# Kernel optimization log

Hardware: AMD Instinct MI355X
Metric: run time of the kernel (lower is better)

## Reference

```python
import jax, jax.numpy as jnp
import numpy as np

BN_EPS = 1e-5
NUM_GRAPHS = 64


def _gin_layer(x, src, dst, eps, w1, b1, gamma, beta, w2, b2):
    # GIN aggregation: sum of source features into destination nodes
    n = x.shape[0]
    agg = jax.ops.segment_sum(x[src], dst, num_segments=n)  # [N, d]
    h = (1.0 + eps) * x + agg
    # MLP: Linear -> BatchNorm1d (batch stats, train mode) -> ReLU -> Linear
    h = h @ w1 + b1
    mu = jnp.mean(h, axis=0)
    var = jnp.var(h, axis=0)
    h = gamma * (h - mu) * jax.lax.rsqrt(var + BN_EPS) + beta
    h = jax.nn.relu(h)
    return h @ w2 + b2


def setup_inputs() -> dict:
    key = jax.random.key(0)
    ks = jax.random.split(key, 16)
    N, E, F = 100000, 3200000, 128
    x = jax.random.normal(ks[0], (N, F), dtype=jnp.float32)
    edge_index = jax.random.randint(ks[1], (2, E), 0, N, dtype=jnp.int64)
    batch = jnp.sort(jax.random.randint(ks[2], (N,), 0, NUM_GRAPHS, dtype=jnp.int64))

    def lin(k, fin, fout):
        kw, kb = jax.random.split(k)
        s = 1.0 / np.sqrt(fin)
        w = jax.random.uniform(kw, (fin, fout), jnp.float32, -s, s)
        b = jax.random.uniform(kb, (fout,), jnp.float32, -s, s)
        return w, b

    w1a, b1a = lin(ks[3], F, 64)
    w1b, b1b = lin(ks[4], 64, 32)
    w2a, b2a = lin(ks[5], 32, 64)
    w2b, b2b = lin(ks[6], 64, 16)
    lw, lb = lin(ks[7], 16, 1)
    return {
        "x": x, "edge_index": edge_index, "batch": batch,
        "eps1": jnp.float32(0.0), "eps2": jnp.float32(0.0),
        "w1a": w1a, "b1a": b1a, "g1": jnp.ones(64, jnp.float32), "bt1": jnp.zeros(64, jnp.float32),
        "w1b": w1b, "b1b": b1b,
        "w2a": w2a, "b2a": b2a, "g2": jnp.ones(64, jnp.float32), "bt2": jnp.zeros(64, jnp.float32),
        "w2b": w2b, "b2b": b2b,
        "lw": lw, "lb": lb,
    }


def reference(x, edge_index, batch, eps1, eps2, w1a, b1a, g1, bt1, w1b, b1b,
              w2a, b2a, g2, bt2, w2b, b2b, lw, lb):
    src, dst = edge_index[0], edge_index[1]
    h = _gin_layer(x, src, dst, eps1, w1a, b1a, g1, bt1, w1b, b1b)   # [N, 32]
    h = _gin_layer(h, src, dst, eps2, w2a, b2a, g2, bt2, w2b, b2b)   # [N, 16]
    # global mean pool over graphs
    sums = jax.ops.segment_sum(h, batch, num_segments=NUM_GRAPHS)    # [G, 16]
    counts = jax.ops.segment_sum(jnp.ones((h.shape[0],), h.dtype), batch,
                                 num_segments=NUM_GRAPHS)
    pooled = sums / jnp.maximum(counts, 1.0)[:, None]
    return jax.nn.sigmoid(pooled @ lw + lb)                           # [G, 1]
```

## Files before the change

kernel.cpp:

```cpp
#include <hip/hip_runtime.h>
#include <hip/hip_fp16.h>
#include <math.h>

#define G_GRAPHS 64
#define BIN_SHIFT 7
#define BIN_SIZE 128
#define NBINS_CAP 1024
#define C_CHUNK 16384

typedef unsigned short usv8 __attribute__((ext_vector_type(8)));

__device__ __forceinline__ void fma4(float4& a, float s, float4 w) {
    a.x += s * w.x; a.y += s * w.y; a.z += s * w.z; a.w += s * w.w;
}
__device__ __forceinline__ void add4(float4& a, float4 b) {
    a.x += b.x; a.y += b.y; a.z += b.z; a.w += b.w;
}
__device__ __forceinline__ float4 h4_to_f4(ushort4 u) {
    return make_float4(__half2float(__ushort_as_half(u.x)),
                       __half2float(__ushort_as_half(u.y)),
                       __half2float(__ushort_as_half(u.z)),
                       __half2float(__ushort_as_half(u.w)));
}
__device__ __forceinline__ ushort4 f4_to_h4(float4 f) {
    ushort4 u;
    u.x = __half_as_ushort(__float2half_rn(f.x));
    u.y = __half_as_ushort(__float2half_rn(f.y));
    u.z = __half_as_ushort(__float2half_rn(f.z));
    u.w = __half_as_ushort(__float2half_rn(f.w));
    return u;
}
__device__ __forceinline__ usv8 f4x2_to_h8(float4 a, float4 b) {
    usv8 r;
    r.s0 = __half_as_ushort(__float2half_rn(a.x));
    r.s1 = __half_as_ushort(__float2half_rn(a.y));
    r.s2 = __half_as_ushort(__float2half_rn(a.z));
    r.s3 = __half_as_ushort(__float2half_rn(a.w));
    r.s4 = __half_as_ushort(__float2half_rn(b.x));
    r.s5 = __half_as_ushort(__float2half_rn(b.y));
    r.s6 = __half_as_ushort(__float2half_rn(b.z));
    r.s7 = __half_as_ushort(__float2half_rn(b.w));
    return r;
}

__device__ __forceinline__ float4 fp8x4_to_f4(unsigned int w) {
#if __has_builtin(__builtin_amdgcn_cvt_f32_fp8)
    float4 r;
    r.x = __builtin_amdgcn_cvt_f32_fp8((int)w, 0);
    r.y = __builtin_amdgcn_cvt_f32_fp8((int)w, 1);
    r.z = __builtin_amdgcn_cvt_f32_fp8((int)w, 2);
    r.w = __builtin_amdgcn_cvt_f32_fp8((int)w, 3);
    return r;
#else
    const float sc = 1.329227995784916e+36f;
    unsigned b0 = w & 0xffu, b1 = (w >> 8) & 0xffu,
             b2 = (w >> 16) & 0xffu, b3 = (w >> 24) & 0xffu;
    float4 r;
    r.x = __uint_as_float(((b0 & 0x80u) << 24) | ((b0 & 0x7fu) << 20)) * sc;
    r.y = __uint_as_float(((b1 & 0x80u) << 24) | ((b1 & 0x7fu) << 20)) * sc;
    r.z = __uint_as_float(((b2 & 0x80u) << 24) | ((b2 & 0x7fu) << 20)) * sc;
    r.w = __uint_as_float(((b3 & 0x80u) << 24) | ((b3 & 0x7fu) << 20)) * sc;
    return r;
#endif
}
__device__ __forceinline__ unsigned int f4_to_fp8x4(float4 f) {
#if __has_builtin(__builtin_amdgcn_cvt_pk_fp8_f32)
    int v = __builtin_amdgcn_cvt_pk_fp8_f32(f.x, f.y, 0, false);
    v = __builtin_amdgcn_cvt_pk_fp8_f32(f.z, f.w, v, true);
    return (unsigned int)v;
#else
    const float sc = 7.52316384526264e-37f;
    float vv[4] = {f.x, f.y, f.z, f.w};
    unsigned out = 0;
    #pragma unroll
    for (int i = 0; i < 4; ++i) {
        unsigned u = __float_as_uint(vv[i] * sc);
        unsigned s = (u >> 24) & 0x80u;
        u += 0x00080000u;
        unsigned m = (u >> 20) & 0x7fu;
        out |= (s | m) << (8 * i);
    }
    return out;
#endif
}

__global__ __launch_bounds__(256) void k_g1A(
    const float* __restrict__ x, const float* __restrict__ w1a,
    unsigned int* __restrict__ y8, int n, int tiles64,
    const int* __restrict__ dst, int* __restrict__ hist, int nE, int nbins,
    int vec4ok)
{
    __shared__ float  xs[64 * 129];
    __shared__ float4 ws[128 * 16];
    __shared__ int    cnt[NBINS_CAP];
    int tid = threadIdx.x;
    if (blockIdx.x < tiles64) {
        const float4* w4 = (const float4*)w1a;
        #pragma unroll
        for (int i = tid; i < 128 * 16; i += 256) ws[i] = w4[i];
        int row0 = blockIdx.x * 64;
        for (int i = tid; i < 64 * 32; i += 256) {
            int r = i >> 5, k4 = i & 31;
            float4 v = {0.f, 0.f, 0.f, 0.f};
            if (row0 + r < n) v = ((const float4*)x)[(size_t)(row0 + r) * 32 + k4];
            xs[r * 129 + k4 * 4 + 0] = v.x;
            xs[r * 129 + k4 * 4 + 1] = v.y;
            xs[r * 129 + k4 * 4 + 2] = v.z;
            xs[r * 129 + k4 * 4 + 3] = v.w;
        }
        __syncthreads();
        int c4 = tid & 15, rg = tid >> 4;
        float4 acc[4] = {{0,0,0,0},{0,0,0,0},{0,0,0,0},{0,0,0,0}};
        const float* xr = xs + rg * 4 * 129;
        #pragma unroll 8
        for (int k = 0; k < 128; ++k) {
            float4 wv = ws[k * 16 + c4];
            fma4(acc[0], xr[k +   0], wv);
            fma4(acc[1], xr[k + 129], wv);
            fma4(acc[2], xr[k + 258], wv);
            fma4(acc[3], xr[k + 387], wv);
        }
        #pragma unroll
        for (int i = 0; i < 4; ++i) {
            int row = row0 + rg * 4 + i;
            if (row < n) y8[(size_t)row * 16 + c4] = f4_to_fp8x4(acc[i]);
        }
    } else {
        int blk = blockIdx.x - tiles64;
        for (int i = tid; i < nbins; i += 256) cnt[i] = 0;
        __syncthreads();
        int base = blk * C_CHUNK;
        int end  = min(base + C_CHUNK, nE);
        int done = base;
        if (vec4ok) {
            int cnt4 = (end - base) >> 2;
            const int4* d4 = (const int4*)(dst + base);
            for (int i = tid; i < cnt4; i += 256) {
                int4 v = d4[i];
                atomicAdd(&cnt[v.x >> BIN_SHIFT], 1);
                atomicAdd(&cnt[v.y >> BIN_SHIFT], 1);
                atomicAdd(&cnt[v.z >> BIN_SHIFT], 1);
                atomicAdd(&cnt[v.w >> BIN_SHIFT], 1);
            }
            done = base + (cnt4 << 2);
        }
        for (int e = done + tid; e < end; e += 256)
            atomicAdd(&cnt[dst[e] >> BIN_SHIFT], 1);
        __syncthreads();
        int* hrow = hist + (size_t)blk * nbins;
        for (int i = tid; i < nbins; i += 256) hrow[i] = cnt[i];
    }
}

__global__ __launch_bounds__(256) void k_binB1(
    int* __restrict__ hist, int cblocks, int nbins, int* __restrict__ binCnt)
{
    __shared__ int sb[256];
    int b = blockIdx.x;
    int t = threadIdx.x;
    int v = (t < cblocks) ? hist[(size_t)t * nbins + b] : 0;
    sb[t] = v;
    __syncthreads();
    for (int d = 1; d < 256; d <<= 1) {
        int tt = (t >= d) ? sb[t - d] : 0;
        __syncthreads();
        sb[t] += tt;
        __syncthreads();
    }
    if (t < cblocks) hist[(size_t)t * nbins + b] = sb[t] - v;
    if (t == 0) binCnt[b] = sb[255];
}

__global__ __launch_bounds__(1024) void k_binB2(
    const int* __restrict__ binCnt, int nbins, int nE,
    int* __restrict__ binOff, int* __restrict__ off, int n)
{
    __shared__ int sb[1024];
    int tid = threadIdx.x;
    int v = (tid < nbins) ? binCnt[tid] : 0;
    sb[tid] = v;
    __syncthreads();
    for (int d = 1; d < 1024; d <<= 1) {
        int t = (tid >= d) ? sb[tid - d] : 0;
        __syncthreads();
        sb[tid] += t;
        __syncthreads();
    }
    if (tid < nbins) binOff[tid] = sb[tid] - v;
    if (tid == 0) { binOff[nbins] = nE; off[n] = nE; }
}

__global__ __launch_bounds__(256) void k_binC2(
    const int* __restrict__ src, const int* __restrict__ dst,
    const int* __restrict__ binOff, const int* __restrict__ hist,
    int* __restrict__ staging, int nE, int nbins, int vec4ok)
{
    __shared__ int cnt[NBINS_CAP];
    const int* hrow = hist + (size_t)blockIdx.x * nbins;
    for (int i = threadIdx.x; i < nbins; i += 256)
        cnt[i] = binOff[i] + hrow[i];
    __syncthreads();
    int base = blockIdx.x * C_CHUNK;
    int end  = min(base + C_CHUNK, nE);
    int done = base;
    if (vec4ok) {
        int cnt4 = (end - base) >> 2;
        const int4* d4 = (const int4*)(dst + base);
        const int4* s4 = (const int4*)(src + base);
        for (int i = threadIdx.x; i < cnt4; i += 256) {
            int4 dv = d4[i]; int4 sv = s4[i];
            int b, p;
            b = dv.x >> BIN_SHIFT; p = atomicAdd(&cnt[b], 1);
            staging[p] = ((dv.x & (BIN_SIZE-1)) << 17) | sv.x;
            b = dv.y >> BIN_SHIFT; p = atomicAdd(&cnt[b], 1);
            staging[p] = ((dv.y & (BIN_SIZE-1)) << 17) | sv.y;
            b = dv.z >> BIN_SHIFT; p = atomicAdd(&cnt[b], 1);
            staging[p] = ((dv.z & (BIN_SIZE-1)) << 17) | sv.z;
            b = dv.w >> BIN_SHIFT; p = atomicAdd(&cnt[b], 1);
            staging[p] = ((dv.w & (BIN_SIZE-1)) << 17) | sv.w;
        }
        done = base + (cnt4 << 2);
    }
    for (int e = done + threadIdx.x; e < end; e += 256) {
        int d = dst[e], s = src[e];
        int b = d >> BIN_SHIFT;
        int p = atomicAdd(&cnt[b], 1);
        staging[p] = ((d & (BIN_SIZE - 1)) << 17) | s;
    }
}

__global__ __launch_bounds__(256) void k_binD(
    const int* __restrict__ binOff, const int* __restrict__ staging,
    int* __restrict__ off, int* __restrict__ csr, int n)
{
    __shared__ int deg[BIN_SIZE];
    __shared__ int cur[BIN_SIZE];
    int b = blockIdx.x;
    int s = binOff[b], e = binOff[b + 1];
    int tid = threadIdx.x;
    if (tid < BIN_SIZE) deg[tid] = 0;
    __syncthreads();
    for (int j = s + tid; j < e; j += 256)
        atomicAdd(&deg[staging[j] >> 17], 1);
    __syncthreads();
    if (tid < BIN_SIZE) cur[tid] = deg[tid];
    __syncthreads();
    for (int d = 1; d < BIN_SIZE; d <<= 1) {
        int t = (tid >= d && tid < BIN_SIZE) ? cur[tid - d] : 0;
        __syncthreads();
        if (tid < BIN_SIZE) cur[tid] += t;
        __syncthreads();
    }
    if (tid < BIN_SIZE) {
        int node = b * BIN_SIZE + tid;
        int ex = s + cur[tid] - deg[tid];
        if (node < n) off[node] = ex;
        cur[tid] = ex;
    }
    __syncthreads();
    for (int j = s + tid; j < e; j += 256) {
        int pk = staging[j];
        int p = atomicAdd(&cur[pk >> 17], 1);
        csr[p] = pk & 0x1FFFF;
    }
}

__global__ __launch_bounds__(256) void k_agg1(
    const unsigned int* __restrict__ y8, const int* __restrict__ off,
    const int* __restrict__ csr, const float* __restrict__ b1a,
    const float* __restrict__ eps1p, __half* __restrict__ h1, int n,
    float* __restrict__ p_sum, float* __restrict__ p_sq)
{
    __shared__ float s_sum[4][64];
    __shared__ float s_sq[4][64];
    int slot = threadIdx.x >> 6;
    int lane = threadIdx.x & 63;
    int node = blockIdx.x * 4 + slot;
    int c = lane & 7;
    int g = lane >> 3;
    bool valid = node < n;
    int o = 0, e = 0;
    if (valid) { o = off[node]; e = off[node + 1]; }
    const uint2* y82 = (const uint2*)y8;
    float4 aLo = {0,0,0,0}, aHi = {0,0,0,0};
    if (valid && g == 0) {
        uint2 v = y82[(size_t)node * 8 + c];
        float4 lo = fp8x4_to_f4(v.x), hi = fp8x4_to_f4(v.y);
        float4 b0 = ((const float4*)b1a)[c * 2];
        float4 b1 = ((const float4*)b1a)[c * 2 + 1];
        float ep = 1.0f + eps1p[0];
        aLo.x = ep * lo.x + b0.x; aLo.y = ep * lo.y + b0.y;
        aLo.z = ep * lo.z + b0.z; aLo.w = ep * lo.w + b0.w;
        aHi.x = ep * hi.x + b1.x; aHi.y = ep * hi.y + b1.y;
        aHi.z = ep * hi.z + b1.z; aHi.w = ep * hi.w + b1.w;
    }
    int j = o + g;
    for (; j + 8 < e; j += 16) {
        int s0 = csr[j], s1 = csr[j + 8];
        uint2 w0 = y82[(size_t)s0 * 8 + c];
        uint2 w1 = y82[(size_t)s1 * 8 + c];
        add4(aLo, fp8x4_to_f4(w0.x)); add4(aHi, fp8x4_to_f4(w0.y));
        add4(aLo, fp8x4_to_f4(w1.x)); add4(aHi, fp8x4_to_f4(w1.y));
    }
    for (; j < e; j += 8) {
        uint2 w = y82[(size_t)csr[j] * 8 + c];
        add4(aLo, fp8x4_to_f4(w.x)); add4(aHi, fp8x4_to_f4(w.y));
    }
    #pragma unroll
    for (int d = 8; d < 64; d <<= 1) {
        aLo.x += __shfl_xor(aLo.x, d, 64); aLo.y += __shfl_xor(aLo.y, d, 64);
        aLo.z += __shfl_xor(aLo.z, d, 64); aLo.w += __shfl_xor(aLo.w, d, 64);
        aHi.x += __shfl_xor(aHi.x, d, 64); aHi.y += __shfl_xor(aHi.y, d, 64);
        aHi.z += __shfl_xor(aHi.z, d, 64); aHi.w += __shfl_xor(aHi.w, d, 64);
    }
    if (g == 0) {
        if (valid) ((usv8*)h1)[(size_t)node * 8 + c] = f4x2_to_h8(aLo, aHi);
        float v0 = valid ? aLo.x : 0.f, v1 = valid ? aLo.y : 0.f;
        float v2 = valid ? aLo.z : 0.f, v3 = valid ? aLo.w : 0.f;
        float v4 = valid ? aHi.x : 0.f, v5 = valid ? aHi.y : 0.f;
        float v6 = valid ? aHi.z : 0.f, v7 = valid ? aHi.w : 0.f;
        s_sum[slot][8*c+0] = v0; s_sum[slot][8*c+1] = v1;
        s_sum[slot][8*c+2] = v2; s_sum[slot][8*c+3] = v3;
        s_sum[slot][8*c+4] = v4; s_sum[slot][8*c+5] = v5;
        s_sum[slot][8*c+6] = v6; s_sum[slot][8*c+7] = v7;
        s_sq[slot][8*c+0] = v0*v0; s_sq[slot][8*c+1] = v1*v1;
        s_sq[slot][8*c+2] = v2*v2; s_sq[slot][8*c+3] = v3*v3;
        s_sq[slot][8*c+4] = v4*v4; s_sq[slot][8*c+5] = v5*v5;
        s_sq[slot][8*c+6] = v6*v6; s_sq[slot][8*c+7] = v7*v7;
    }
    __syncthreads();
    if (threadIdx.x < 64) {
        int col = threadIdx.x;
        float s = s_sum[0][col] + s_sum[1][col] + s_sum[2][col] + s_sum[3][col];
        float q = s_sq[0][col]  + s_sq[1][col]  + s_sq[2][col]  + s_sq[3][col];
        int ps = (blockIdx.x & 63) * 64 + col;
        atomicAdd(&p_sum[ps], s);
        atomicAdd(&p_sq[ps], q);
    }
}

__global__ __launch_bounds__(256) void k_agg2(
    const unsigned int* __restrict__ h28, const int* __restrict__ off,
    const int* __restrict__ csr, const float* __restrict__ eps2p,
    __half* __restrict__ agg2h, int n)
{
    int node = blockIdx.x * 4 + (threadIdx.x >> 6);
    if (node >= n) return;
    int lane = threadIdx.x & 63;
    int c = lane & 3;
    int g = lane >> 2;
    int o = off[node], e = off[node + 1];
    const uint2* h282 = (const uint2*)h28;
    float4 aLo = {0,0,0,0}, aHi = {0,0,0,0};
    if (g == 0) {
        uint2 v = h282[(size_t)node * 4 + c];
        float4 lo = fp8x4_to_f4(v.x), hi = fp8x4_to_f4(v.y);
        float ep = 1.0f + eps2p[0];
        aLo.x = ep * lo.x; aLo.y = ep * lo.y; aLo.z = ep * lo.z; aLo.w = ep * lo.w;
        aHi.x = ep * hi.x; aHi.y = ep * hi.y; aHi.z = ep * hi.z; aHi.w = ep * hi.w;
    }
    int j = o + g;
    for (; j + 16 < e; j += 32) {
        int s0 = csr[j], s1 = csr[j + 16];
        uint2 w0 = h282[(size_t)s0 * 4 + c];
        uint2 w1 = h282[(size_t)s1 * 4 + c];
        add4(aLo, fp8x4_to_f4(w0.x)); add4(aHi, fp8x4_to_f4(w0.y));
        add4(aLo, fp8x4_to_f4(w1.x)); add4(aHi, fp8x4_to_f4(w1.y));
    }
    for (; j < e; j += 16) {
        uint2 w = h282[(size_t)csr[j] * 4 + c];
        add4(aLo, fp8x4_to_f4(w.x)); add4(aHi, fp8x4_to_f4(w.y));
    }
    #pragma unroll
    for (int d = 4; d < 64; d <<= 1) {
        aLo.x += __shfl_xor(aLo.x, d, 64); aLo.y += __shfl_xor(aLo.y, d, 64);
        aLo.z += __shfl_xor(aLo.z, d, 64); aLo.w += __shfl_xor(aLo.w, d, 64);
        aHi.x += __shfl_xor(aHi.x, d, 64); aHi.y += __shfl_xor(aHi.y, d, 64);
        aHi.z += __shfl_xor(aHi.z, d, 64); aHi.w += __shfl_xor(aHi.w, d, 64);
    }
    if (g == 0)
        ((usv8*)agg2h)[(size_t)node * 4 + c] = f4x2_to_h8(aLo, aHi);
}

__global__ void k_bnfin(const float* __restrict__ p_sum, const float* __restrict__ p_sq,
                        const float* __restrict__ gamma, const float* __restrict__ beta,
                        float nf, float* __restrict__ a, float* __restrict__ c)
{
    int i = threadIdx.x;
    float s = 0.f, q = 0.f;
    for (int k = 0; k < 64; ++k) { s += p_sum[k*64 + i]; q += p_sq[k*64 + i]; }
    float mu  = s / nf;
    float var = q / nf - mu * mu;
    float av  = gamma[i] * rsqrtf(var + 1e-5f);
    a[i] = av;
    c[i] = beta[i] - av * mu;
}

__global__ __launch_bounds__(256) void k_mlp1b(
    const __half* __restrict__ h1, const float* __restrict__ a1,
    const float* __restrict__ c1, const float* __restrict__ w1b,
    const float* __restrict__ b1b, unsigned int* __restrict__ h28, int n)
{
    __shared__ float  xs[128 * 65];
    __shared__ float4 ws[64 * 8];
    __shared__ float  as[64], cs[64];
    int tid = threadIdx.x;
    #pragma unroll
    for (int i = tid; i < 64 * 8; i += 256) ws[i] = ((const float4*)w1b)[i];
    if (tid < 64) { as[tid] = a1[tid]; cs[tid] = c1[tid]; }
    __syncthreads();
    int row0 = blockIdx.x * 128;
    for (int i = tid; i < 128 * 16; i += 256) {
        int r = i >> 4, k4 = i & 15;
        float4 v = {0.f, 0.f, 0.f, 0.f};
        if (row0 + r < n) {
            v = h4_to_f4(((const ushort4*)h1)[(size_t)(row0 + r) * 16 + k4]);
            v.x = fmaxf(as[k4*4+0] * v.x + cs[k4*4+0], 0.f);
            v.y = fmaxf(as[k4*4+1] * v.y + cs[k4*4+1], 0.f);
            v.z = fmaxf(as[k4*4+2] * v.z + cs[k4*4+2], 0.f);
            v.w = fmaxf(as[k4*4+3] * v.w + cs[k4*4+3], 0.f);
        }
        xs[r * 65 + k4 * 4 + 0] = v.x;
        xs[r * 65 + k4 * 4 + 1] = v.y;
        xs[r * 65 + k4 * 4 + 2] = v.z;
        xs[r * 65 + k4 * 4 + 3] = v.w;
    }
    __syncthreads();
    int c4 = tid & 7, rg = tid >> 3;
    float4 bv = ((const float4*)b1b)[c4];
    float4 acc[4] = {bv, bv, bv, bv};
    const float* xr = xs + rg * 4 * 65;
    #pragma unroll 8
    for (int k = 0; k < 64; ++k) {
        float4 wv = ws[k * 8 + c4];
        fma4(acc[0], xr[k +   0], wv);
        fma4(acc[1], xr[k +  65], wv);
        fma4(acc[2], xr[k + 130], wv);
        fma4(acc[3], xr[k + 195], wv);
    }
    #pragma unroll
    for (int i = 0; i < 4; ++i) {
        int row = row0 + rg * 4 + i;
        if (row < n) h28[(size_t)row * 8 + c4] = f4_to_fp8x4(acc[i]);
    }
}

__global__ __launch_bounds__(256) void k_gemm2(
    const __half* __restrict__ agg2h, const float* __restrict__ w2a,
    const float* __restrict__ b2a, __half* __restrict__ h3, int n,
    float* __restrict__ p_sum, float* __restrict__ p_sq)
{
    __shared__ float  xs[64 * 33];
    __shared__ float4 ws[32 * 16];
    __shared__ float  s_sum[64], s_sq[64];
    int tid = threadIdx.x;
    if (tid < 64) { s_sum[tid] = 0.f; s_sq[tid] = 0.f; }
    #pragma unroll
    for (int i = tid; i < 32 * 16; i += 256) ws[i] = ((const float4*)w2a)[i];
    int row0 = blockIdx.x * 64;
    for (int i = tid; i < 64 * 8; i += 256) {
        int r = i >> 3, k4 = i & 7;
        float4 v = {0.f, 0.f, 0.f, 0.f};
        if (row0 + r < n) v = h4_to_f4(((const ushort4*)agg2h)[(size_t)(row0 + r) * 8 + k4]);
        xs[r * 33 + k4 * 4 + 0] = v.x;
        xs[r * 33 + k4 * 4 + 1] = v.y;
        xs[r * 33 + k4 * 4 + 2] = v.z;
        xs[r * 33 + k4 * 4 + 3] = v.w;
    }
    __syncthreads();
    int c4 = tid & 15, rg = tid >> 4;
    float4 bv = ((const float4*)b2a)[c4];
    float4 acc[4] = {bv, bv, bv, bv};
    const float* xr = xs + rg * 4 * 33;
    #pragma unroll
    for (int k = 0; k < 32; ++k) {
        float4 wv = ws[k * 16 + c4];
        fma4(acc[0], xr[k +  0], wv);
        fma4(acc[1], xr[k + 33], wv);
        fma4(acc[2], xr[k + 66], wv);
        fma4(acc[3], xr[k + 99], wv);
    }
    float cs_[4] = {0,0,0,0}, cq_[4] = {0,0,0,0};
    #pragma unroll
    for (int i = 0; i < 4; ++i) {
        int row = row0 + rg * 4 + i;
        if (row < n) {
            ((ushort4*)h3)[(size_t)row * 16 + c4] = f4_to_h4(acc[i]);
            cs_[0] += acc[i].x; cq_[0] += acc[i].x * acc[i].x;
            cs_[1] += acc[i].y; cq_[1] += acc[i].y * acc[i].y;
            cs_[2] += acc[i].z; cq_[2] += acc[i].z * acc[i].z;
            cs_[3] += acc[i].w; cq_[3] += acc[i].w * acc[i].w;
        }
    }
    #pragma unroll
    for (int jj = 0; jj < 4; ++jj) {
        atomicAdd(&s_sum[c4 * 4 + jj], cs_[jj]);
        atomicAdd(&s_sq[c4 * 4 + jj],  cq_[jj]);
    }
    __syncthreads();
    if (tid < 64) {
        int ps = (blockIdx.x & 63) * 64 + tid;
        atomicAdd(&p_sum[ps], s_sum[tid]);
        atomicAdd(&p_sq[ps],  s_sq[tid]);
    }
}

__global__ __launch_bounds__(256) void k_final(
    const __half* __restrict__ h3, const float* __restrict__ a2,
    const float* __restrict__ c2, const float* __restrict__ w2b,
    const float* __restrict__ b2b, const int* __restrict__ batch,
    float* __restrict__ pool, float* __restrict__ cnt, int n)
{
    __shared__ float  xs[64 * 65];
    __shared__ float4 ws[64 * 4];
    __shared__ float  as[64], cs[64];
    __shared__ float  pl[G_GRAPHS * 16];
    __shared__ float  cl[G_GRAPHS];
    int tid = threadIdx.x;
    for (int i = tid; i < 256; i += 256) ws[i] = ((const float4*)w2b)[i];
    if (tid < 64) { as[tid] = a2[tid]; cs[tid] = c2[tid]; cl[tid] = 0.f; }
    for (int i = tid; i < G_GRAPHS * 16; i += 256) pl[i] = 0.f;
    __syncthreads();
    int row0 = blockIdx.x * 64;
    for (int i = tid; i < 64 * 16; i += 256) {
        int r = i >> 4, k4 = i & 15;
        float4 v = {0.f, 0.f, 0.f, 0.f};
        if (row0 + r < n) {
            v = h4_to_f4(((const ushort4*)h3)[(size_t)(row0 + r) * 16 + k4]);
            v.x = fmaxf(as[k4*4+0] * v.x + cs[k4*4+0], 0.f);
            v.y = fmaxf(as[k4*4+1] * v.y + cs[k4*4+1], 0.f);
            v.z = fmaxf(as[k4*4+2] * v.z + cs[k4*4+2], 0.f);
            v.w = fmaxf(as[k4*4+3] * v.w + cs[k4*4+3], 0.f);
        }
        xs[r * 65 + k4 * 4 + 0] = v.x;
        xs[r * 65 + k4 * 4 + 1] = v.y;
        xs[r * 65 + k4 * 4 + 2] = v.z;
        xs[r * 65 + k4 * 4 + 3] = v.w;
    }
    __syncthreads();
    int c4 = tid & 3, r = tid >> 2;
    float4 acc = ((const float4*)b2b)[c4];
    const float* xr = xs + r * 65;
    #pragma unroll 8
    for (int k = 0; k < 64; ++k) {
        float4 wv = ws[k * 4 + c4];
        fma4(acc, xr[k], wv);
    }
    int row = row0 + r;
    if (row < n) {
        int g = batch[row];
        if (c4 == 0) atomicAdd(&cl[g], 1.f);
        float* pp = &pl[g * 16 + c4 * 4];
        atomicAdd(pp + 0, acc.x); atomicAdd(pp + 1, acc.y);
        atomicAdd(pp + 2, acc.z); atomicAdd(pp + 3, acc.w);
    }
    __syncthreads();
    if (tid < 64 && cl[tid] != 0.f) atomicAdd(&cnt[tid], cl[tid]);
    for (int i = tid; i < G_GRAPHS * 16; i += 256) {
        int g = i >> 4;
        if (cl[g] != 0.f) atomicAdd(&pool[i], pl[i]);
    }
}

__global__ void k_head(const float* __restrict__ pool, const float* __restrict__ cnt,
                       const float* __restrict__ lw, const float* __restrict__ lb,
                       float* __restrict__ out)
{
    int g = threadIdx.x;
    float cv = fmaxf(cnt[g], 1.0f);
    float acc = lb[0];
    #pragma unroll
    for (int f = 0; f < 16; ++f) acc += (pool[g * 16 + f] / cv) * lw[f];
    out[g] = 1.0f / (1.0f + expf(-acc));
}

extern "C" void kernel_launch(void* const* d_in, const int* in_sizes, int n_in,
                              void* d_out, int out_size, void* d_ws, size_t ws_size,
                              hipStream_t stream)
{
    const float* x    = (const float*)d_in[0];
    const int*   eidx = (const int*)d_in[1];
    const int*   batch= (const int*)d_in[2];
    const float* eps1 = (const float*)d_in[3];
    const float* eps2 = (const float*)d_in[4];
    const float* w1a  = (const float*)d_in[5];
    const float* b1a  = (const float*)d_in[6];
    const float* g1   = (const float*)d_in[7];
    const float* bt1  = (const float*)d_in[8];
    const float* w1b  = (const float*)d_in[9];
    const float* b1b  = (const float*)d_in[10];
    const float* w2a  = (const float*)d_in[11];
    const float* b2a  = (const float*)d_in[12];
    const float* g2   = (const float*)d_in[13];
    const float* bt2  = (const float*)d_in[14];
    const float* w2b  = (const float*)d_in[15];
    const float* b2b  = (const float*)d_in[16];
    const float* lw   = (const float*)d_in[17];
    const float* lb   = (const float*)d_in[18];
    float* out = (float*)d_out;

    int n  = in_sizes[0] / 128;
    int nE = in_sizes[1] / 2;
    const int* srcI = eidx;
    const int* dstI = eidx + nE;
    int vec4ok = ((nE & 3) == 0) && ((((uintptr_t)eidx) & 15) == 0);

    char* wsb = (char*)d_ws;
    size_t nn = (size_t)n;
    unsigned int* y8  = (unsigned int*)wsb;
    __half* h1        = (__half*)(wsb + nn * 64);
    unsigned int* h28 = (unsigned int*)(wsb + nn * 192);
    __half* agg2h     = (__half*)(wsb + nn * 224);
    __half* h3        = h1;
    float* stats = (float*)(wsb + nn * 288);
    float* a1     = stats;          float* c1     = stats + 64;
    float* a2     = stats + 128;    float* c2     = stats + 192;
    float* pool   = stats + 256;    float* cntb   = stats + 1280;
    float* p_sum1 = stats + 1344;   float* p_sq1  = stats + 5440;
    float* p_sum2 = stats + 9536;   float* p_sq2  = stats + 13632;

    int cblocks = (nE + C_CHUNK - 1) / C_CHUNK;
    int nbins   = (n + BIN_SIZE - 1) >> BIN_SHIFT;

    int* off     = (int*)(stats + 17728);
    int* csr     = off + (n + 1);
    int* binCnt  = csr + nE;
    int* binOff  = binCnt + NBINS_CAP + 1;
    int* staging = binOff + NBINS_CAP + 1;
    int* hist    = staging + nE;

    hipMemsetAsync(stats + 256, 0, (17728 - 256) * sizeof(float), stream);

    int tiles64  = (n + 63) / 64;
    int tiles128 = (n + 127) / 128;
    int nblocks4 = (n + 3) / 4;

    k_g1A<<<tiles64 + cblocks, 256, 0, stream>>>(x, w1a, y8, n, tiles64,
                                                 dstI, hist, nE, nbins, vec4ok);
    k_binB1<<<nbins, 256, 0, stream>>>(hist, cblocks, nbins, binCnt);
    k_binB2<<<1, 1024, 0, stream>>>(binCnt, nbins, nE, binOff, off, n);
    k_binC2<<<cblocks, 256, 0, stream>>>(srcI, dstI, binOff, hist, staging, nE, nbins, vec4ok);
    k_binD<<<nbins, 256, 0, stream>>>(binOff, staging, off, csr, n);

    k_agg1<<<nblocks4, 256, 0, stream>>>(y8, off, csr, b1a, eps1, h1, n, p_sum1, p_sq1);
    k_bnfin<<<1, 64, 0, stream>>>(p_sum1, p_sq1, g1, bt1, (float)n, a1, c1);
    k_mlp1b<<<tiles128, 256, 0, stream>>>(h1, a1, c1, w1b, b1b, h28, n);
    k_agg2<<<nblocks4, 256, 0, stream>>>(h28, off, csr, eps2, agg2h, n);
    k_gemm2<<<tiles64, 256, 0, stream>>>(agg2h, w2a, b2a, h3, n, p_sum2, p_sq2);
    k_bnfin<<<1, 64, 0, stream>>>(p_sum2, p_sq2, g2, bt2, (float)n, a2, c2);
    k_final<<<tiles64, 256, 0, stream>>>(h3, a2, c2, w2b, b2b, batch, pool, cntb, n);
    k_head<<<1, 64, 0, stream>>>(pool, cntb, lw, lb, out);
}
```

Baseline: 278.0 us.

## Fuse per-bin CSR build into aggregation kernels using shared-memory local CSR

Removes the separate k_binD kernel and the global off/csr arrays. Each aggregation kernel now takes one 128-node bin per 512-thread block, builds that bin's CSR in LDS from the staging buffer, then aggregates neighbors. If a bin has more edges than LDS can hold, it falls back to a global buffer. In layer 1 the neighbor sums are split into two passes by source half (source index below n/2, then above), which looks aimed at locality of the y8 gathers, with a partial sum held in LDS. This saves a kernel launch and the global CSR write and read, but the CSR build is repeated in both aggregation kernels, grid parallelism drops to about 782 large blocks, and the large LDS footprint may lower occupancy.

```diff
diff --git a/kernel.cpp b/kernel.cpp
--- a/kernel.cpp
+++ b/kernel.cpp
@@ -7,6 +7,7 @@
 #define BIN_SIZE 128
 #define NBINS_CAP 1024
 #define C_CHUNK 16384
+#define CAP 4608
 
 typedef unsigned short usv8 __attribute__((ext_vector_type(8)));
 
@@ -172,8 +173,7 @@
 }
 
 __global__ __launch_bounds__(1024) void k_binB2(
-    const int* __restrict__ binCnt, int nbins, int nE,
-    int* __restrict__ binOff, int* __restrict__ off, int n)
+    const int* __restrict__ binCnt, int nbins, int nE, int* __restrict__ binOff)
 {
     __shared__ int sb[1024];
     int tid = threadIdx.x;
@@ -187,7 +187,7 @@
         __syncthreads();
     }
     if (tid < nbins) binOff[tid] = sb[tid] - v;
-    if (tid == 0) { binOff[nbins] = nE; off[n] = nE; }
+    if (tid == 0) binOff[nbins] = nE;
 }
 
 __global__ __launch_bounds__(256) void k_binC2(
@@ -229,21 +229,196 @@
     }
 }
 
-__global__ __launch_bounds__(256) void k_binD(
-    const int* __restrict__ binOff, const int* __restrict__ staging,
-    int* __restrict__ off, int* __restrict__ csr, int n)
-{
-    __shared__ int deg[BIN_SIZE];
-    __shared__ int cur[BIN_SIZE];
+__global__ __launch_bounds__(512) void k_agg1(
+    const unsigned int* __restrict__ y8, const int* __restrict__ binOff,
+    const int* __restrict__ staging, int* __restrict__ csr_fb,
+    const float* __restrict__ b1a, const float* __restrict__ eps1p,
+    __half* __restrict__ h1, int n,
+    float* __restrict__ p_sum, float* __restrict__ p_sq)
+{
+    __shared__ int   stage_s[CAP];
+    __shared__ int   lcsr_s[CAP];
+    __shared__ int   degA[BIN_SIZE], degT[BIN_SIZE];
+    __shared__ int   start_[BIN_SIZE], curA[BIN_SIZE], curB[BIN_SIZE];
+    __shared__ float s_sum[8][64], s_sq[8][64];
+    usv8* acch = (usv8*)stage_s;
+
     int b = blockIdx.x;
     int s = binOff[b], e = binOff[b + 1];
+    int cntE = e - s;
     int tid = threadIdx.x;
-    if (tid < BIN_SIZE) deg[tid] = 0;
-    __syncthreads();
-    for (int j = s + tid; j < e; j += 256)
-        atomicAdd(&deg[staging[j] >> 17], 1);
-    __syncthreads();
-    if (tid < BIN_SIZE) cur[tid] = deg[tid];
+    bool fits = (cntE <= CAP);
+    int nHalf = n >> 1;
+
+    if (tid < BIN_SIZE) { degA[tid] = 0; degT[tid] = 0; }
+    __syncthreads();
+    for (int j = tid; j < cntE; j += 512) {
+        int pk = staging[s + j];
+        if (fits) stage_s[j] = pk;
+        int ln = pk >> 17;
+        atomicAdd(&degT[ln], 1);
+        if ((pk & 0x1FFFF) < nHalf) atomicAdd(&degA[ln], 1);
+    }
+    __syncthreads();
+    if (tid < BIN_SIZE) curA[tid] = degT[tid];
+    __syncthreads();
+    for (int d = 1; d < BIN_SIZE; d <<= 1) {
+        int t = (tid >= d && tid < BIN_SIZE) ? curA[tid - d] : 0;
+        __syncthreads();
+        if (tid < BIN_SIZE) curA[tid] += t;
+        __syncthreads();
+    }
+    if (tid < BIN_SIZE) {
+        int st = curA[tid] - degT[tid];
+        start_[tid] = st;
+        curA[tid] = st;
+        curB[tid] = st + degA[tid];
+    }
+    __syncthreads();
+    int* lcsr = fits ? lcsr_s : (csr_fb + s);
+    for (int j = tid; j < cntE; j += 512) {
+        int pk = fits ? stage_s[j] : staging[s + j];
+        int ln = pk >> 17, sv = pk & 0x1FFFF;
+        int p = (sv < nHalf) ? atomicAdd(&curA[ln], 1) : atomicAdd(&curB[ln], 1);
+        lcsr[p] = sv;
+    }
+    __syncthreads();
+
+    int wave = tid >> 6, lane = tid & 63;
+    int c = lane & 7, g = lane >> 3;
+    const uint2* y82 = (const uint2*)y8;
+    float ep = 1.0f + eps1p[0];
+    float4 bv0 = ((const float4*)b1a)[c * 2];
+    float4 bv1 = ((const float4*)b1a)[c * 2 + 1];
+    int node0 = b * BIN_SIZE;
+
+    for (int k = 0; k < 16; ++k) {
+        int ln = wave * 16 + k;
+        int node = node0 + ln;
+        if (node >= n) break;
+        int o  = start_[ln];
+        int eA = o + degA[ln];
+        float4 aLo = {0,0,0,0}, aHi = {0,0,0,0};
+        if (g == 0) {
+            uint2 v = y82[(size_t)node * 8 + c];
+            float4 lo = fp8x4_to_f4(v.x), hi = fp8x4_to_f4(v.y);
+            aLo.x = ep * lo.x + bv0.x; aLo.y = ep * lo.y + bv0.y;
+            aLo.z = ep * lo.z + bv0.z; aLo.w = ep * lo.w + bv0.w;
+            aHi.x = ep * hi.x + bv1.x; aHi.y = ep * hi.y + bv1.y;
+            aHi.z = ep * hi.z + bv1.z; aHi.w = ep * hi.w + bv1.w;
+        }
+        int j = o + g;
+        for (; j + 8 < eA; j += 16) {
+            int s0 = lcsr[j], s1 = lcsr[j + 8];
+            uint2 w0 = y82[(size_t)s0 * 8 + c];
+            uint2 w1 = y82[(size_t)s1 * 8 + c];
+            add4(aLo, fp8x4_to_f4(w0.x)); add4(aHi, fp8x4_to_f4(w0.y));
+            add4(aLo, fp8x4_to_f4(w1.x)); add4(aHi, fp8x4_to_f4(w1.y));
+        }
+        for (; j < eA; j += 8) {
+            uint2 w = y82[(size_t)lcsr[j] * 8 + c];
+            add4(aLo, fp8x4_to_f4(w.x)); add4(aHi, fp8x4_to_f4(w.y));
+        }
+        #pragma unroll
+        for (int d = 8; d < 64; d <<= 1) {
+            aLo.x += __shfl_xor(aLo.x, d, 64); aLo.y += __shfl_xor(aLo.y, d, 64);
+            aLo.z += __shfl_xor(aLo.z, d, 64); aLo.w += __shfl_xor(aLo.w, d, 64);
+            aHi.x += __shfl_xor(aHi.x, d, 64); aHi.y += __shfl_xor(aHi.y, d, 64);
+            aHi.z += __shfl_xor(aHi.z, d, 64); aHi.w += __shfl_xor(aHi.w, d, 64);
+        }
+        if (g == 0) acch[ln * 8 + c] = f4x2_to_h8(aLo, aHi);
+    }
+    __syncthreads();
+
+    float rs[8] = {0,0,0,0,0,0,0,0}, rq[8] = {0,0,0,0,0,0,0,0};
+    for (int k = 0; k < 16; ++k) {
+        int ln = wave * 16 + k;
+        int node = node0 + ln;
+        if (node >= n) break;
+        int o  = start_[ln];
+        int eA = o + degA[ln];
+        int eT = o + degT[ln];
+        float4 aLo = {0,0,0,0}, aHi = {0,0,0,0};
+        int j = eA + g;
+        for (; j + 8 < eT; j += 16) {
+            int s0 = lcsr[j], s1 = lcsr[j + 8];
+            uint2 w0 = y82[(size_t)s0 * 8 + c];
+            uint2 w1 = y82[(size_t)s1 * 8 + c];
+            add4(aLo, fp8x4_to_f4(w0.x)); add4(aHi, fp8x4_to_f4(w0.y));
+            add4(aLo, fp8x4_to_f4(w1.x)); add4(aHi, fp8x4_to_f4(w1.y));
+        }
+        for (; j < eT; j += 8) {
+            uint2 w = y82[(size_t)lcsr[j] * 8 + c];
+            add4(aLo, fp8x4_to_f4(w.x)); add4(aHi, fp8x4_to_f4(w.y));
+        }
+        #pragma unroll
+        for (int d = 8; d < 64; d <<= 1) {
+            aLo.x += __shfl_xor(aLo.x, d, 64); aLo.y += __shfl_xor(aLo.y, d, 64);
+            aLo.z += __shfl_xor(aLo.z, d, 64); aLo.w += __shfl_xor(aLo.w, d, 64);
+            aHi.x += __shfl_xor(aHi.x, d, 64); aHi.y += __shfl_xor(aHi.y, d, 64);
+            aHi.z += __shfl_xor(aHi.z, d, 64); aHi.w += __shfl_xor(aHi.w, d, 64);
+        }
+        if (g == 0) {
+            usv8 ph = acch[ln * 8 + c];
+            aLo.x += __half2float(__ushort_as_half(ph.s0));
+            aLo.y += __half2float(__ushort_as_half(ph.s1));
+            aLo.z += __half2float(__ushort_as_half(ph.s2));
+            aLo.w += __half2float(__ushort_as_half(ph.s3));
+            aHi.x += __half2float(__ushort_as_half(ph.s4));
+            aHi.y += __half2float(__ushort_as_half(ph.s5));
+            aHi.z += __half2float(__ushort_as_half(ph.s6));
+            aHi.w += __half2float(__ushort_as_half(ph.s7));
+            ((usv8*)h1)[(size_t)node * 8 + c] = f4x2_to_h8(aLo, aHi);
+            rs[0] += aLo.x; rq[0] += aLo.x * aLo.x;
+            rs[1] += aLo.y; rq[1] += aLo.y * aLo.y;
+            rs[2] += aLo.z; rq[2] += aLo.z * aLo.z;
+            rs[3] += aLo.w; rq[3] += aLo.w * aLo.w;
+            rs[4] += aHi.x; rq[4] += aHi.x * aHi.x;
+            rs[5] += aHi.y; rq[5] += aHi.y * aHi.y;
+            rs[6] += aHi.z; rq[6] += aHi.z * aHi.z;
+            rs[7] += aHi.w; rq[7] += aHi.w * aHi.w;
+        }
+    }
+    if (g == 0) {
+        #pragma unroll
+        for (int i = 0; i < 8; ++i) {
+            s_sum[wave][8 * c + i] = rs[i];
+            s_sq[wave][8 * c + i]  = rq[i];
+        }
+    }
+    __syncthreads();
+    if (tid < 64) {
+        float ssum = 0.f, ssq = 0.f;
+        #pragma unroll
+        for (int w = 0; w < 8; ++w) { ssum += s_sum[w][tid]; ssq += s_sq[w][tid]; }
+        int ps = (b & 63) * 64 + tid;
+        atomicAdd(&p_sum[ps], ssum);
+        atomicAdd(&p_sq[ps], ssq);
+    }
+}
+
+__global__ __launch_bounds__(512) void k_agg2(
+    const unsigned int* __restrict__ h28, const int* __restrict__ binOff,
+    const int* __restrict__ staging, int* __restrict__ csr_fb,
+    const float* __restrict__ eps2p, __half* __restrict__ agg2h, int n)
+{
+    __shared__ int stage_s[CAP];
+    __shared__ int lcsr_s[CAP];
+    __shared__ int degT[BIN_SIZE], start_[BIN_SIZE], cur[BIN_SIZE];
+    int b = blockIdx.x;
+    int s = binOff[b], e = binOff[b + 1];
+    int cntE = e - s;
+    int tid = threadIdx.x;
+    bool fits = (cntE <= CAP);
+    if (tid < BIN_SIZE) degT[tid] = 0;
+    __syncthreads();
+    for (int j = tid; j < cntE; j += 512) {
+        int pk = staging[s + j];
+        if (fits) stage_s[j] = pk;
+        atomicAdd(&degT[pk >> 17], 1);
+    }
+    __syncthreads();
+    if (tid < BIN_SIZE) cur[tid] = degT[tid];
     __syncthreads();
     for (int d = 1; d < BIN_SIZE; d <<= 1) {
         int t = (tid >= d && tid < BIN_SIZE) ? cur[tid - d] : 0;
@@ -252,134 +427,58 @@
         __syncthreads();
     }
     if (tid < BIN_SIZE) {
-        int node = b * BIN_SIZE + tid;
-        int ex = s + cur[tid] - deg[tid];
-        if (node < n) off[node] = ex;
-        cur[tid] = ex;
-    }
-    __syncthreads();
-    for (int j = s + tid; j < e; j += 256) {
-        int pk = staging[j];
+        int st = cur[tid] - degT[tid];
+        start_[tid] = st;
+        cur[tid] = st;
+    }
+    __syncthreads();
+    int* lcsr = fits ? lcsr_s : (csr_fb + s);
+    for (int j = tid; j < cntE; j += 512) {
+        int pk = fits ? stage_s[j] : staging[s + j];
         int p = atomicAdd(&cur[pk >> 17], 1);
-        csr[p] = pk & 0x1FFFF;
-    }
-}
-
-__global__ __launch_bounds__(256) void k_agg1(
-    const unsigned int* __restrict__ y8, const int* __restrict__ off,
-    const int* __restrict__ csr, const float* __restrict__ b1a,
-    const float* __restrict__ eps1p, __half* __restrict__ h1, int n,
-    float* __restrict__ p_sum, float* __restrict__ p_sq)
-{
-    __shared__ float s_sum[4][64];
-    __shared__ float s_sq[4][64];
-    int slot = threadIdx.x >> 6;
-    int lane = threadIdx.x & 63;
-    int node = blockIdx.x * 4 + slot;
-    int c = lane & 7;
-    int g = lane >> 3;
-    bool valid = node < n;
-    int o = 0, e = 0;
-    if (valid) { o = off[node]; e = off[node + 1]; }
-    const uint2* y82 = (const uint2*)y8;
-    float4 aLo = {0,0,0,0}, aHi = {0,0,0,0};
-    if (valid && g == 0) {
-        uint2 v = y82[(size_t)node * 8 + c];
-        float4 lo = fp8x4_to_f4(v.x), hi = fp8x4_to_f4(v.y);
-        float4 b0 = ((const float4*)b1a)[c * 2];
-        float4 b1 = ((const float4*)b1a)[c * 2 + 1];
-        float ep = 1.0f + eps1p[0];
-        aLo.x = ep * lo.x + b0.x; aLo.y = ep * lo.y + b0.y;
-        aLo.z = ep * lo.z + b0.z; aLo.w = ep * lo.w + b0.w;
-        aHi.x = ep * hi.x + b1.x; aHi.y = ep * hi.y + b1.y;
-        aHi.z = ep * hi.z + b1.z; aHi.w = ep * hi.w + b1.w;
-    }
-    int j = o + g;
-    for (; j + 8 < e; j += 16) {
-        int s0 = csr[j], s1 = csr[j + 8];
-        uint2 w0 = y82[(size_t)s0 * 8 + c];
-        uint2 w1 = y82[(size_t)s1 * 8 + c];
-        add4(aLo, fp8x4_to_f4(w0.x)); add4(aHi, fp8x4_to_f4(w0.y));
-        add4(aLo, fp8x4_to_f4(w1.x)); add4(aHi, fp8x4_to_f4(w1.y));
-    }
-    for (; j < e; j += 8) {
-        uint2 w = y82[(size_t)csr[j] * 8 + c];
-        add4(aLo, fp8x4_to_f4(w.x)); add4(aHi, fp8x4_to_f4(w.y));
-    }
-    #pragma unroll
-    for (int d = 8; d < 64; d <<= 1) {
-        aLo.x += __shfl_xor(aLo.x, d, 64); aLo.y += __shfl_xor(aLo.y, d, 64);
-        aLo.z += __shfl_xor(aLo.z, d, 64); aLo.w += __shfl_xor(aLo.w, d, 64);
-        aHi.x += __shfl_xor(aHi.x, d, 64); aHi.y += __shfl_xor(aHi.y, d, 64);
-        aHi.z += __shfl_xor(aHi.z, d, 64); aHi.w += __shfl_xor(aHi.w, d, 64);
-    }
-    if (g == 0) {
-        if (valid) ((usv8*)h1)[(size_t)node * 8 + c] = f4x2_to_h8(aLo, aHi);
-        float v0 = valid ? aLo.x : 0.f, v1 = valid ? aLo.y : 0.f;
-        float v2 = valid ? aLo.z : 0.f, v3 = valid ? aLo.w : 0.f;
-        float v4 = valid ? aHi.x : 0.f, v5 = valid ? aHi.y : 0.f;
-        float v6 = valid ? aHi.z : 0.f, v7 = valid ? aHi.w : 0.f;
-        s_sum[slot][8*c+0] = v0; s_sum[slot][8*c+1] = v1;
-        s_sum[slot][8*c+2] = v2; s_sum[slot][8*c+3] = v3;
-        s_sum[slot][8*c+4] = v4; s_sum[slot][8*c+5] = v5;
-        s_sum[slot][8*c+6] = v6; s_sum[slot][8*c+7] = v7;
-        s_sq[slot][8*c+0] = v0*v0; s_sq[slot][8*c+1] = v1*v1;
-        s_sq[slot][8*c+2] = v2*v2; s_sq[slot][8*c+3] = v3*v3;
-        s_sq[slot][8*c+4] = v4*v4; s_sq[slot][8*c+5] = v5*v5;
-        s_sq[slot][8*c+6] = v6*v6; s_sq[slot][8*c+7] = v7*v7;
-    }
-    __syncthreads();
-    if (threadIdx.x < 64) {
-        int col = threadIdx.x;
-        float s = s_sum[0][col] + s_sum[1][col] + s_sum[2][col] + s_sum[3][col];
-        float q = s_sq[0][col]  + s_sq[1][col]  + s_sq[2][col]  + s_sq[3][col];
-        int ps = (blockIdx.x & 63) * 64 + col;
-        atomicAdd(&p_sum[ps], s);
-        atomicAdd(&p_sq[ps], q);
-    }
-}
-
-__global__ __launch_bounds__(256) void k_agg2(
-    const unsigned int* __restrict__ h28, const int* __restrict__ off,
-    const int* __restrict__ csr, const float* __restrict__ eps2p,
-    __half* __restrict__ agg2h, int n)
-{
-    int node = blockIdx.x * 4 + (threadIdx.x >> 6);
-    if (node >= n) return;
-    int lane = threadIdx.x & 63;
-    int c = lane & 3;
-    int g = lane >> 2;
-    int o = off[node], e = off[node + 1];
+        lcsr[p] = pk & 0x1FFFF;
+    }
+    __syncthreads();
+
+    int wave = tid >> 6, lane = tid & 63;
+    int c = lane & 3, g = lane >> 2;
     const uint2* h282 = (const uint2*)h28;
-    float4 aLo = {0,0,0,0}, aHi = {0,0,0,0};
-    if (g == 0) {
-        uint2 v = h282[(size_t)node * 4 + c];
-        float4 lo = fp8x4_to_f4(v.x), hi = fp8x4_to_f4(v.y);
-        float ep = 1.0f + eps2p[0];
-        aLo.x = ep * lo.x; aLo.y = ep * lo.y; aLo.z = ep * lo.z; aLo.w = ep * lo.w;
-        aHi.x = ep * hi.x; aHi.y = ep * hi.y; aHi.z = ep * hi.z; aHi.w = ep * hi.w;
-    }
-    int j = o + g;
-    for (; j + 16 < e; j += 32) {
-        int s0 = csr[j], s1 = csr[j + 16];
-        uint2 w0 = h282[(size_t)s0 * 4 + c];
-        uint2 w1 = h282[(size_t)s1 * 4 + c];
-        add4(aLo, fp8x4_to_f4(w0.x)); add4(aHi, fp8x4_to_f4(w0.y));
-        add4(aLo, fp8x4_to_f4(w1.x)); add4(aHi, fp8x4_to_f4(w1.y));
-    }
-    for (; j < e; j += 16) {
-        uint2 w = h282[(size_t)csr[j] * 4 + c];
-        add4(aLo, fp8x4_to_f4(w.x)); add4(aHi, fp8x4_to_f4(w.y));
-    }
-    #pragma unroll
-    for (int d = 4; d < 64; d <<= 1) {
-        aLo.x += __shfl_xor(aLo.x, d, 64); aLo.y += __shfl_xor(aLo.y, d, 64);
-        aLo.z += __shfl_xor(aLo.z, d, 64); aLo.w += __shfl_xor(aLo.w, d, 64);
-        aHi.x += __shfl_xor(aHi.x, d, 64); aHi.y += __shfl_xor(aHi.y, d, 64);
-        aHi.z += __shfl_xor(aHi.z, d, 64); aHi.w += __shfl_xor(aHi.w, d, 64);
-    }
-    if (g == 0)
-        ((usv8*)agg2h)[(size_t)node * 4 + c] = f4x2_to_h8(aLo, aHi);
+    float ep = 1.0f + eps2p[0];
+    int node0 = b * BIN_SIZE;
+    for (int k = 0; k < 16; ++k) {
+        int ln = wave * 16 + k;
+        int node = node0 + ln;
+        if (node >= n) break;
+        int o = start_[ln], eT = o + degT[ln];
+        float4 aLo = {0,0,0,0}, aHi = {0,0,0,0};
+        if (g == 0) {
+            uint2 v = h282[(size_t)node * 4 + c];
+            float4 lo = fp8x4_to_f4(v.x), hi = fp8x4_to_f4(v.y);
+            aLo.x = ep * lo.x; aLo.y = ep * lo.y; aLo.z = ep * lo.z; aLo.w = ep * lo.w;
+            aHi.x = ep * hi.x; aHi.y = ep * hi.y; aHi.z = ep * hi.z; aHi.w = ep * hi.w;
+        }
+        int j = o + g;
+        for (; j + 16 < eT; j += 32) {
+            int s0 = lcsr[j], s1 = lcsr[j + 16];
+            uint2 w0 = h282[(size_t)s0 * 4 + c];
+            uint2 w1 = h282[(size_t)s1 * 4 + c];
+            add4(aLo, fp8x4_to_f4(w0.x)); add4(aHi, fp8x4_to_f4(w0.y));
+            add4(aLo, fp8x4_to_f4(w1.x)); add4(aHi, fp8x4_to_f4(w1.y));
+        }
+        for (; j < eT; j += 16) {
+            uint2 w = h282[(size_t)lcsr[j] * 4 + c];
+            add4(aLo, fp8x4_to_f4(w.x)); add4(aHi, fp8x4_to_f4(w.y));
+        }
+        #pragma unroll
+        for (int d = 4; d < 64; d <<= 1) {
+            aLo.x += __shfl_xor(aLo.x, d, 64); aLo.y += __shfl_xor(aLo.y, d, 64);
+            aLo.z += __shfl_xor(aLo.z, d, 64); aLo.w += __shfl_xor(aLo.w, d, 64);
+            aHi.x += __shfl_xor(aHi.x, d, 64); aHi.y += __shfl_xor(aHi.y, d, 64);
+            aHi.z += __shfl_xor(aHi.z, d, 64); aHi.w += __shfl_xor(aHi.w, d, 64);
+        }
+        if (g == 0)
+            ((usv8*)agg2h)[(size_t)node * 4 + c] = f4x2_to_h8(aLo, aHi);
+    }
 }
 
 __global__ void k_bnfin(const float* __restrict__ p_sum, const float* __restrict__ p_sq,
@@ -622,30 +721,27 @@
     int cblocks = (nE + C_CHUNK - 1) / C_CHUNK;
     int nbins   = (n + BIN_SIZE - 1) >> BIN_SHIFT;
 
-    int* off     = (int*)(stats + 17728);
-    int* csr     = off + (n + 1);
-    int* binCnt  = csr + nE;
+    int* binCnt  = (int*)(stats + 17728);
     int* binOff  = binCnt + NBINS_CAP + 1;
     int* staging = binOff + NBINS_CAP + 1;
     int* hist    = staging + nE;
+    int* csr_fb  = hist + (size_t)cblocks * nbins;
 
     hipMemsetAsync(stats + 256, 0, (17728 - 256) * sizeof(float), stream);
 
     int tiles64  = (n + 63) / 64;
     int tiles128 = (n + 127) / 128;
-    int nblocks4 = (n + 3) / 4;
 
     k_g1A<<<tiles64 + cblocks, 256, 0, stream>>>(x, w1a, y8, n, tiles64,
                                                  dstI, hist, nE, nbins, vec4ok);
     k_binB1<<<nbins, 256, 0, stream>>>(hist, cblocks, nbins, binCnt);
-    k_binB2<<<1, 1024, 0, stream>>>(binCnt, nbins, nE, binOff, off, n);
+    k_binB2<<<1, 1024, 0, stream>>>(binCnt, nbins, nE, binOff);
     k_binC2<<<cblocks, 256, 0, stream>>>(srcI, dstI, binOff, hist, staging, nE, nbins, vec4ok);
-    k_binD<<<nbins, 256, 0, stream>>>(binOff, staging, off, csr, n);
-
-    k_agg1<<<nblocks4, 256, 0, stream>>>(y8, off, csr, b1a, eps1, h1, n, p_sum1, p_sq1);
+
+    k_agg1<<<nbins, 512, 0, stream>>>(y8, binOff, staging, csr_fb, b1a, eps1, h1, n, p_sum1, p_sq1);
     k_bnfin<<<1, 64, 0, stream>>>(p_sum1, p_sq1, g1, bt1, (float)n, a1, c1);
     k_mlp1b<<<tiles128, 256, 0, stream>>>(h1, a1, c1, w1b, b1b, h28, n);
-    k_agg2<<<nblocks4, 256, 0, stream>>>(h28, off, csr, eps2, agg2h, n);
+    k_agg2<<<nbins, 512, 0, stream>>>(h28, binOff, staging, csr_fb, eps2, agg2h, n);
     k_gemm2<<<tiles64, 256, 0, stream>>>(agg2h, w2a, b2a, h3, n, p_sum2, p_sq2);
     k_bnfin<<<1, 64, 0, stream>>>(p_sum2, p_sq2, g2, bt2, (float)n, a2, c2);
     k_final<<<tiles64, 256, 0, stream>>>(h3, a2, c2, w2b, b2b, batch, pool, cntb, n);
```

After: 327.8 us. 17.9% more time.
